# Optimization experiments

Measured on AMD Instinct MI355X. Metric: run time of the kernel, lower is better.

The kernel has to match this reference:

```python
import jax, jax.numpy as jnp
import numpy as np

N, E, IN, HID, H, G, CLS = 20000, 160000, 128, 96, 6, 512, 128
HD = H * HID  # heads * out_channels = 576
ARC_S = 30.0  # ArcFace scale (no margin at inference, no labels passed)


def _lin_params(key, fan_in, fan_out):
    k1, k2 = jax.random.split(key)
    lim = 1.0 / np.sqrt(fan_in)
    W = jax.random.uniform(k1, (fan_in, fan_out), minval=-lim, maxval=lim, dtype=jnp.float32)
    b = jax.random.uniform(k2, (fan_out,), minval=-lim, maxval=lim, dtype=jnp.float32)
    return W, b


def setup_inputs() -> dict:
    key = jax.random.key(0)
    ks = jax.random.split(key, 32)
    x = jax.random.normal(ks[0], (N, IN), dtype=jnp.float32)
    edge_index = jax.random.randint(ks[1], (2, E), 0, N, dtype=jnp.int64)
    batch = jnp.sort(jax.random.randint(ks[2], (N,), 0, G, dtype=jnp.int64))
    # conv1: IN -> HID (per-head dim HID, H heads)
    Wq1, bq1 = _lin_params(ks[3], IN, HD)
    Wk1, bk1 = _lin_params(ks[4], IN, HD)
    Wv1, bv1 = _lin_params(ks[5], IN, HD)
    Ws1, bs1 = _lin_params(ks[6], IN, HID)
    # convs 2..5 share shapes: HID -> HID, stacked on leading axis of 4
    def stack(fn_keys, fi, fo):
        Ws, bs = zip(*[_lin_params(k, fi, fo) for k in fn_keys])
        return jnp.stack(Ws), jnp.stack(bs)
    Wq_r, bq_r = stack(ks[7:11], HID, HD)
    Wk_r, bk_r = stack(ks[11:15], HID, HD)
    Wv_r, bv_r = stack(ks[15:19], HID, HD)
    Ws_r, bs_r = stack(ks[19:23], HID, HID)
    fc1_w, fc1_b = _lin_params(ks[23], HID, HID)
    fc2_w, fc2_b = _lin_params(ks[24], HID, HID)
    arc_w = jax.random.normal(ks[25], (CLS, HID), dtype=jnp.float32)
    return dict(x=x, edge_index=edge_index, batch=batch,
                Wq1=Wq1, bq1=bq1, Wk1=Wk1, bk1=bk1, Wv1=Wv1, bv1=bv1, Ws1=Ws1, bs1=bs1,
                Wq_r=Wq_r, bq_r=bq_r, Wk_r=Wk_r, bk_r=bk_r, Wv_r=Wv_r, bv_r=bv_r,
                Ws_r=Ws_r, bs_r=bs_r,
                fc1_w=fc1_w, fc1_b=fc1_b, fc2_w=fc2_w, fc2_b=fc2_b, arc_w=arc_w)


def transformer_conv(x, src, dst, Wq, bq, Wk, bk, Wv, bv, Ws, bs):
    n = x.shape[0]
    q = (x @ Wq + bq).reshape(n, H, HID)
    k = (x @ Wk + bk).reshape(n, H, HID)
    v = (x @ Wv + bv).reshape(n, H, HID)
    # edge-wise attention logits [E, H]
    alpha = jnp.einsum('ehd,ehd->eh', q[dst], k[src]) / jnp.sqrt(jnp.float32(HID))
    # segment softmax over incoming edges of each destination node
    m = jax.ops.segment_max(alpha, dst, num_segments=n)
    a = jnp.exp(alpha - m[dst])
    s = jax.ops.segment_sum(a, dst, num_segments=n)
    a = a / s[dst]
    out = jax.ops.segment_sum(a[:, :, None] * v[src], dst, num_segments=n)  # [n, H, HID]
    # concat=False -> mean over heads; root_weight skip connection
    return out.mean(axis=1) + x @ Ws + bs


def reference(x, edge_index, batch,
              Wq1, bq1, Wk1, bk1, Wv1, bv1, Ws1, bs1,
              Wq_r, bq_r, Wk_r, bk_r, Wv_r, bv_r, Ws_r, bs_r,
              fc1_w, fc1_b, fc2_w, fc2_b, arc_w):
    src, dst = edge_index[0], edge_index[1]
    h = jax.nn.relu(transformer_conv(x, src, dst, Wq1, bq1, Wk1, bk1, Wv1, bv1, Ws1, bs1))
    for i in range(4):  # gtconv2..gtconv5
        h = jax.nn.relu(transformer_conv(h, src, dst, Wq_r[i], bq_r[i], Wk_r[i], bk_r[i],
                                         Wv_r[i], bv_r[i], Ws_r[i], bs_r[i]))
    # global mean pool over graphs
    sums = jax.ops.segment_sum(h, batch, num_segments=G)
    cnt = jax.ops.segment_sum(jnp.ones((h.shape[0], 1), h.dtype), batch, num_segments=G)
    g = sums / jnp.maximum(cnt, 1.0)
    g = jax.nn.relu(g @ fc1_w + fc1_b)
    g = jax.nn.relu(g @ fc2_w + fc2_b)
    # ArcFace without labels: scaled cosine logits
    gn = g / (jnp.linalg.norm(g, axis=-1, keepdims=True) + 1e-12)
    wn = arc_w / (jnp.linalg.norm(arc_w, axis=-1, keepdims=True) + 1e-12)
    return ARC_S * (gn @ wn.T)
```

## Files before the change

### kernel.cpp

```cpp
#include <hip/hip_runtime.h>
#include <math.h>

#define N_NODES 20000
#define N_EDGES 160000
#define DIM_IN  128
#define HIDDEN  96
#define NH      6
#define HD      576
#define LDROW   704
#define KVF8LD  1152
#define NALL    1824
#define NGRAPH  512
#define NCLS    128
#define CHUNK   32
#define SLD     104
#define BSTR    112

typedef unsigned short ushort_t;
typedef unsigned char uchar_t;
typedef __attribute__((ext_vector_type(8))) short bf16x8;
typedef __attribute__((ext_vector_type(4))) float f32x4;
typedef __attribute__((ext_vector_type(2))) float f32x2;

static __device__ __forceinline__ ushort_t f2bf(float f) {
    unsigned int u = __float_as_uint(f);
    return (ushort_t)((u + 0x7fffu + ((u >> 16) & 1u)) >> 16);
}
static __device__ __forceinline__ float bfs(ushort_t u) { return __uint_as_float((unsigned int)u << 16); }
static __device__ __forceinline__ float bflo(unsigned int u) { return __uint_as_float(u << 16); }
static __device__ __forceinline__ float bfhi(unsigned int u) { return __uint_as_float(u & 0xffff0000u); }

__global__ void k_cvt(const float* __restrict__ src, ushort_t* __restrict__ dst, int n)
{
    int i = blockIdx.x * blockDim.x + threadIdx.x;
    if (i < n) dst[i] = f2bf(src[i]);
}

__global__ void k_cvt_wT_all(
    const float* __restrict__ Wq1, const float* __restrict__ Wk1,
    const float* __restrict__ Wv1, const float* __restrict__ Ws1,
    const float* __restrict__ Wq_r, const float* __restrict__ Wk_r,
    const float* __restrict__ Wv_r, const float* __restrict__ Ws_r,
    ushort_t* __restrict__ Wb0, ushort_t* __restrict__ Wbr)
{
    const int L = blockIdx.y;
    const int K = (L == 0) ? DIM_IN : HIDDEN;
    int i = blockIdx.x * blockDim.x + threadIdx.x;
    if (i >= K * NALL) return;
    const float *Wq, *Wk, *Wv, *Ws; ushort_t* dst;
    if (L == 0) { Wq = Wq1; Wk = Wk1; Wv = Wv1; Ws = Ws1; dst = Wb0; }
    else {
        int j = L - 1;
        Wq = Wq_r + (size_t)j * HIDDEN * HD; Wk = Wk_r + (size_t)j * HIDDEN * HD;
        Wv = Wv_r + (size_t)j * HIDDEN * HD; Ws = Ws_r + (size_t)j * HIDDEN * HIDDEN;
        dst = Wbr + (size_t)j * HIDDEN * NALL;
    }
    int n = i / K, k = i - n * K;
    float v;
    if (n < 576)       v = Wq[(size_t)k * HD + n];
    else if (n < 1152) v = Wk[(size_t)k * HD + (n - 576)];
    else if (n < 1728) v = Wv[(size_t)k * HD + (n - 1152)];
    else               v = Ws[(size_t)k * HIDDEN + (n - 1728)];
    dst[i] = f2bf(v);
}

template<int KDIM>
__global__ __launch_bounds__(256) void gemm_qkvs_mfma(
    const ushort_t* __restrict__ A, int M,
    const ushort_t* __restrict__ WbT,
    const float* __restrict__ bq, const float* __restrict__ bk,
    const float* __restrict__ bv, const float* __restrict__ bs,
    ushort_t* __restrict__ kvqs, uchar_t* __restrict__ kvf8)
{
    constexpr int LDB = KDIM + 8;
    constexpr int K8  = KDIM >> 3;
    __shared__ __align__(16) ushort_t smem[128 * SLD];
    const int t    = threadIdx.x;
    const int lane = t & 63;
    const int w    = t >> 6;
    const int wm   = w & 1, wn = w >> 1;
    const int quad = lane >> 4;
    const int l16  = lane & 15;
    const int m0   = blockIdx.y * 128;
    const int rb   = blockIdx.x;
    const int n0   = rb * 96;

    for (int idx = t; idx < 96 * K8; idx += 256) {
        int c = idx / K8, kc = idx - c * K8;
        uint4 v = *(const uint4*)(WbT + (size_t)(n0 + c) * KDIM + kc * 8);
        *(uint4*)(&smem[c * LDB + kc * 8]) = v;
    }

    const ushort_t* Arow[4];
    #pragma unroll
    for (int i = 0; i < 4; i++) {
        int row = m0 + wm * 64 + i * 16 + l16;
        row = min(row, M - 1);
        Arow[i] = A + (size_t)row * KDIM + quad * 8;
    }
    __syncthreads();

    f32x4 acc[4][3] = {};
    #pragma unroll
    for (int ks = 0; ks < KDIM; ks += 32) {
        bf16x8 af[4], bfv[3];
        #pragma unroll
        for (int i = 0; i < 4; i++) af[i] = *(const bf16x8*)(Arow[i] + ks);
        #pragma unroll
        for (int j = 0; j < 3; j++)
            bfv[j] = *(const bf16x8*)(&smem[(wn * 48 + j * 16 + l16) * LDB + ks + quad * 8]);
        #pragma unroll
        for (int i = 0; i < 4; i++)
            #pragma unroll
            for (int j = 0; j < 3; j++)
                acc[i][j] = __builtin_amdgcn_mfma_f32_16x16x32_bf16(af[i], bfv[j], acc[i][j], 0, 0, 0);
    }

    int region; const float* biasp;
    if (rb < 6)       { region = 0; biasp = bq; }
    else if (rb < 12) { region = 1; biasp = bk; }
    else if (rb < 18) { region = 2; biasp = bv; }
    else              { region = 3; biasp = bs; }
    const int colbase = (region == 3) ? 0 : (rb - region * 6) * 96;
    float bj[3];
    #pragma unroll
    for (int j = 0; j < 3; j++) bj[j] = biasp[colbase + wn * 48 + j * 16 + l16];

    __syncthreads();

    if (region == 1 || region == 2) {
        uchar_t* bstage = (uchar_t*)smem;
        #pragma unroll
        for (int i = 0; i < 4; i++) {
            #pragma unroll
            for (int r = 0; r < 4; r++) {
                int row = wm * 64 + i * 16 + quad * 4 + r;
                #pragma unroll
                for (int j = 0; j < 3; j++) {
                    float v = acc[i][j][r] + bj[j];
                    int pk = __builtin_amdgcn_cvt_pk_fp8_f32(v, v, 0, false);
                    bstage[row * BSTR + wn * 48 + j * 16 + l16] = (uchar_t)(pk & 0xff);
                }
            }
        }
        __syncthreads();
        const int c0 = (rb - 6) * 96;
        for (int idx = t; idx < 128 * 6; idx += 256) {
            int r = idx / 6, v4 = idx - r * 6;
            int row = m0 + r;
            if (row < M)
                *(uint4*)(kvf8 + (size_t)row * KVF8LD + c0 + v4 * 16) =
                    *(const uint4*)(bstage + r * BSTR + v4 * 16);
        }
    } else {
        int dstoff = (region == 0) ? n0 : 576;
        #pragma unroll
        for (int i = 0; i < 4; i++) {
            #pragma unroll
            for (int r = 0; r < 4; r++) {
                int row = wm * 64 + i * 16 + quad * 4 + r;
                #pragma unroll
                for (int j = 0; j < 3; j++)
                    smem[row * SLD + wn * 48 + j * 16 + l16] = f2bf(acc[i][j][r] + bj[j]);
            }
        }
        __syncthreads();
        for (int idx = t; idx < 128 * 12; idx += 256) {
            int r = idx / 12, v = idx - r * 12;
            int row = m0 + r;
            if (row < M)
                *(uint4*)(kvqs + (size_t)row * LDROW + dstoff + v * 8) =
                    *(const uint4*)(&smem[r * SLD + v * 8]);
        }
    }
}

__global__ void k_deg(const int* __restrict__ edst, int* __restrict__ deg)
{
    int e = blockIdx.x * blockDim.x + threadIdx.x;
    if (e < N_EDGES) atomicAdd(&deg[edst[e]], 1);
}

__global__ __launch_bounds__(1024) void k_scan(const int* __restrict__ deg,
                                               int* __restrict__ row_ptr,
                                               int* __restrict__ cursor)
{
    __shared__ int part[1024];
    int t = threadIdx.x;
    const int chunk = (N_NODES + 1023) / 1024;
    int b = t * chunk;
    int s = 0;
    for (int i = 0; i < chunk; i++)
        if (b + i < N_NODES) s += deg[b + i];
    part[t] = s;
    __syncthreads();
    for (int o = 1; o < 1024; o <<= 1) {
        int v = (t >= o) ? part[t - o] : 0;
        __syncthreads();
        part[t] += v;
        __syncthreads();
    }
    int run = part[t] - s;
    for (int i = 0; i < chunk; i++) {
        if (b + i < N_NODES) {
            row_ptr[b + i] = run;
            cursor[b + i]  = run;
            run += deg[b + i];
        }
    }
    if (t == 1023) row_ptr[N_NODES] = part[1023];
}

__global__ void k_scatter(const int* __restrict__ esrc, const int* __restrict__ edst,
                          int* __restrict__ cursor, int* __restrict__ csrc)
{
    int e = blockIdx.x * blockDim.x + threadIdx.x;
    if (e < N_EDGES) {
        int pos = atomicAdd(&cursor[edst[e]], 1);
        csrc[pos] = esrc[e];
    }
}

__global__ void k_gbound(const int* __restrict__ batch, int* __restrict__ gbound)
{
    int g = blockIdx.x * blockDim.x + threadIdx.x;
    if (g > NGRAPH) return;
    int lo = 0, hi = N_NODES;
    while (lo < hi) {
        int mid = (lo + hi) >> 1;
        if (batch[mid] < g) lo = mid + 1; else hi = mid;
    }
    gbound[g] = lo;
}

__global__ __launch_bounds__(192) void node_attn(
    const ushort_t* __restrict__ kvqs, const uchar_t* __restrict__ kvf8,
    const int* __restrict__ row_ptr, const int* __restrict__ csrc,
    ushort_t* __restrict__ hb, float* __restrict__ hf)
{
    const int n = blockIdx.x;
    const int t = threadIdx.x;
    const int lane = t & 31;
    const int g = t >> 5;
    const int el = lane >> 2;
    const int qr = lane & 3;

    __shared__ float Qs[HD];
    __shared__ float wbuf[CHUNK * NH];
    __shared__ int   srcs[CHUNK];
    __shared__ float m[NH], l[NH], scale[NH], linv[NH];
    __shared__ float arr[HD];

    const int beg = row_ptr[n], end = row_ptr[n + 1];
    const ushort_t* qk = kvqs + (size_t)n * LDROW;

    if (t < 72) {
        uint4 v = *(const uint4*)(qk + t * 8);
        unsigned int uu[4] = {v.x, v.y, v.z, v.w};
        #pragma unroll
        for (int j = 0; j < 4; j++) {
            Qs[t * 8 + 2 * j]     = bflo(uu[j]);
            Qs[t * 8 + 2 * j + 1] = bfhi(uu[j]);
        }
    }
    if (t < NH) { m[t] = -1e30f; l[t] = 0.f; }

    const int d4 = 4 * t;
    const int hh = d4 / HIDDEN;
    float a[4] = {0.f, 0.f, 0.f, 0.f};
    const float qa = 0.10206207261596577f;
    const uchar_t* vbase = kvf8 + 576 + d4;

    for (int cb = beg; cb < end; cb += CHUNK) {
        const int c = min(CHUNK, end - cb);
        __syncthreads();
        if (t < c) srcs[t] = csrc[cb + t];
        __syncthreads();

        for (int eb = 0; eb < c; eb += 8) {
            int e8 = eb + el;
            bool act = e8 < c;
            int src = srcs[act ? e8 : 0];
            const uchar_t* kp = kvf8 + (size_t)src * KVF8LD + g * HIDDEN + qr * 24;
            uint2 a0 = *(const uint2*)(kp);
            uint2 a1 = *(const uint2*)(kp + 8);
            uint2 a2 = *(const uint2*)(kp + 16);
            const float* qb = &Qs[g * HIDDEN + qr * 24];
            unsigned int uu[6] = {a0.x, a0.y, a1.x, a1.y, a2.x, a2.y};
            float p = 0.f;
            #pragma unroll
            for (int k2 = 0; k2 < 6; k2++) {
                f32x2 lo = __builtin_amdgcn_cvt_pk_f32_fp8(uu[k2], false);
                f32x2 hi = __builtin_amdgcn_cvt_pk_f32_fp8(uu[k2], true);
                p += lo[0] * qb[4 * k2]     + lo[1] * qb[4 * k2 + 1]
                   + hi[0] * qb[4 * k2 + 2] + hi[1] * qb[4 * k2 + 3];
            }
            p += __shfl_xor(p, 1, 32);
            p += __shfl_xor(p, 2, 32);
            if (act && qr == 0) wbuf[e8 * NH + g] = p * qa;
        }
        __syncthreads();

        {
            float logit = (lane < c) ? wbuf[lane * NH + g] : -1e30f;
            float cm = logit;
            #pragma unroll
            for (int o = 16; o; o >>= 1) cm = fmaxf(cm, __shfl_xor(cm, o, 32));
            cm = fmaxf(cm, m[g]);
            float wv = (lane < c) ? __expf(logit - cm) : 0.f;
            if (lane < c) wbuf[lane * NH + g] = wv;
            float lp = wv;
            #pragma unroll
            for (int o = 16; o; o >>= 1) lp += __shfl_xor(lp, o, 32);
            if (lane == 0) {
                float sc = __expf(m[g] - cm);
                scale[g] = sc;
                l[g] = l[g] * sc + lp;
                m[g] = cm;
            }
        }
        __syncthreads();

        if (t < 144) {
            float sc = scale[hh];
            #pragma unroll
            for (int j = 0; j < 4; j++) a[j] *= sc;
            int e = 0;
            for (; e + 4 <= c; e += 4) {
                unsigned int r[4];
                #pragma unroll
                for (int j = 0; j < 4; j++)
                    r[j] = *(const unsigned int*)(vbase + (size_t)srcs[e + j] * KVF8LD);
                #pragma unroll
                for (int j = 0; j < 4; j++) {
                    float w2 = wbuf[(e + j) * NH + hh];
                    f32x2 lo = __builtin_amdgcn_cvt_pk_f32_fp8(r[j], false);
                    f32x2 hi = __builtin_amdgcn_cvt_pk_f32_fp8(r[j], true);
                    a[0] += w2 * lo[0];
                    a[1] += w2 * lo[1];
                    a[2] += w2 * hi[0];
                    a[3] += w2 * hi[1];
                }
            }
            for (; e < c; e++) {
                unsigned int r = *(const unsigned int*)(vbase + (size_t)srcs[e] * KVF8LD);
                float w2 = wbuf[e * NH + hh];
                f32x2 lo = __builtin_amdgcn_cvt_pk_f32_fp8(r, false);
                f32x2 hi = __builtin_amdgcn_cvt_pk_f32_fp8(r, true);
                a[0] += w2 * lo[0];
                a[1] += w2 * lo[1];
                a[2] += w2 * hi[0];
                a[3] += w2 * hi[1];
            }
        }
    }

    if (t < NH) linv[t] = (l[t] > 0.f) ? 1.0f / l[t] : 0.f;
    __syncthreads();
    if (t < 144) {
        float li = linv[hh];
        #pragma unroll
        for (int j = 0; j < 4; j++) arr[d4 + j] = a[j] * li;
    }
    __syncthreads();

    if (t < HIDDEN) {
        float s = (arr[t] + arr[HIDDEN + t] + arr[2 * HIDDEN + t] +
                   arr[3 * HIDDEN + t] + arr[4 * HIDDEN + t] + arr[5 * HIDDEN + t])
                  * (1.0f / 6.0f);
        s += bfs(qk[576 + t]);
        s = fmaxf(s, 0.0f);
        hb[n * HIDDEN + t] = f2bf(s);
        hf[n * HIDDEN + t] = s;
    }
}

__global__ __launch_bounds__(128) void k_head(
    const float* __restrict__ hf, const int* __restrict__ gbound,
    const float* __restrict__ fc1w, const float* __restrict__ fc1b,
    const float* __restrict__ fc2w, const float* __restrict__ fc2b,
    const float* __restrict__ arcw, float* __restrict__ out)
{
    int g = blockIdx.x, t = threadIdx.x;
    __shared__ float v0[HIDDEN], v1[HIDDEN], v2[HIDDEN];
    __shared__ float gnorm;
    const int s0 = gbound[g], s1 = gbound[g + 1];
    float cnt = fmaxf((float)(s1 - s0), 1.0f);
    if (t < HIDDEN) {
        float s = 0.f;
        for (int n = s0; n < s1; n++) s += hf[(size_t)n * HIDDEN + t];
        v0[t] = s / cnt;
    }
    __syncthreads();
    if (t < HIDDEN) {
        float s = fc1b[t];
        for (int k = 0; k < HIDDEN; k++) s += v0[k] * fc1w[k * HIDDEN + t];
        v1[t] = fmaxf(s, 0.f);
    }
    __syncthreads();
    if (t < HIDDEN) {
        float s = fc2b[t];
        for (int k = 0; k < HIDDEN; k++) s += v1[k] * fc2w[k * HIDDEN + t];
        v2[t] = fmaxf(s, 0.f);
    }
    __syncthreads();
    if (t == 0) {
        float s = 0.f;
        for (int k = 0; k < HIDDEN; k++) s += v2[k] * v2[k];
        gnorm = sqrtf(s) + 1e-12f;
    }
    __syncthreads();
    if (t < NCLS) {
        float dot = 0.f, wn = 0.f;
        const float* wr = arcw + (size_t)t * HIDDEN;
        for (int k = 0; k < HIDDEN; k++) {
            float w = wr[k];
            dot += w * v2[k];
            wn  += w * w;
        }
        out[g * NCLS + t] = 30.0f * dot / (gnorm * (sqrtf(wn) + 1e-12f));
    }
}

extern "C" void kernel_launch(void* const* d_in, const int* in_sizes, int n_in,
                              void* d_out, int out_size, void* d_ws, size_t ws_size,
                              hipStream_t stream)
{
    (void)in_sizes; (void)n_in; (void)out_size; (void)ws_size;

    const float* x     = (const float*)d_in[0];
    const int*   ei    = (const int*)d_in[1];
    const int*   batch = (const int*)d_in[2];
    const float* Wq1 = (const float*)d_in[3];  const float* bq1 = (const float*)d_in[4];
    const float* Wk1 = (const float*)d_in[5];  const float* bk1 = (const float*)d_in[6];
    const float* Wv1 = (const float*)d_in[7];  const float* bv1 = (const float*)d_in[8];
    const float* Ws1 = (const float*)d_in[9];  const float* bs1 = (const float*)d_in[10];
    const float* Wq_r = (const float*)d_in[11]; const float* bq_r = (const float*)d_in[12];
    const float* Wk_r = (const float*)d_in[13]; const float* bk_r = (const float*)d_in[14];
    const float* Wv_r = (const float*)d_in[15]; const float* bv_r = (const float*)d_in[16];
    const float* Ws_r = (const float*)d_in[17]; const float* bs_r = (const float*)d_in[18];
    const float* fc1w = (const float*)d_in[19]; const float* fc1b = (const float*)d_in[20];
    const float* fc2w = (const float*)d_in[21]; const float* fc2b = (const float*)d_in[22];
    const float* arcw = (const float*)d_in[23];
    float* out = (float*)d_out;

    const int* esrc = ei;
    const int* edst = ei + N_EDGES;

    char* base = (char*)d_ws;
    size_t off = 0;
    auto alloc = [&](size_t bytes) -> void* {
        off = (off + 255) & ~(size_t)255;
        void* p = base + off;
        off += bytes;
        return p;
    };
    ushort_t* kvqs = (ushort_t*)alloc((size_t)N_NODES * LDROW * 2);
    uchar_t*  kvf8 = (uchar_t*)alloc((size_t)N_NODES * KVF8LD);
    ushort_t* xb  = (ushort_t*)alloc((size_t)N_NODES * DIM_IN * 2);
    ushort_t* hb0 = (ushort_t*)alloc((size_t)N_NODES * HIDDEN * 2);
    ushort_t* hb1 = (ushort_t*)alloc((size_t)N_NODES * HIDDEN * 2);
    float*    hf  = (float*)alloc((size_t)N_NODES * HIDDEN * 4);
    ushort_t* Wb0 = (ushort_t*)alloc((size_t)DIM_IN * NALL * 2);
    ushort_t* Wbr = (ushort_t*)alloc((size_t)4 * HIDDEN * NALL * 2);
    int*   deg     = (int*)alloc(N_NODES * 4);
    int*   row_ptr = (int*)alloc((N_NODES + 1) * 4);
    int*   cursor  = (int*)alloc(N_NODES * 4);
    int*   csrc    = (int*)alloc(N_EDGES * 4);
    int*   gbound  = (int*)alloc((NGRAPH + 1) * 4);

    k_cvt<<<(N_NODES * DIM_IN + 255) / 256, 256, 0, stream>>>(x, xb, N_NODES * DIM_IN);
    {
        dim3 gw((DIM_IN * NALL + 255) / 256, 5);
        k_cvt_wT_all<<<gw, 256, 0, stream>>>(Wq1, Wk1, Wv1, Ws1,
                                             Wq_r, Wk_r, Wv_r, Ws_r, Wb0, Wbr);
    }

    hipMemsetAsync(deg, 0, N_NODES * 4, stream);
    k_deg<<<(N_EDGES + 255) / 256, 256, 0, stream>>>(edst, deg);
    k_scan<<<1, 1024, 0, stream>>>(deg, row_ptr, cursor);
    k_scatter<<<(N_EDGES + 255) / 256, 256, 0, stream>>>(esrc, edst, cursor, csrc);
    k_gbound<<<(NGRAPH + 1 + 255) / 256, 256, 0, stream>>>(batch, gbound);

    const ushort_t* Ain = xb;
    ushort_t* hbcur = hb0;
    for (int L = 0; L < 5; L++) {
        const ushort_t* Wb = (L == 0) ? Wb0 : (Wbr + (size_t)(L - 1) * HIDDEN * NALL);
        const float *bq, *bk, *bv, *bs;
        if (L == 0) { bq = bq1; bk = bk1; bv = bv1; bs = bs1; }
        else {
            int i = L - 1;
            bq = bq_r + (size_t)i * HD; bk = bk_r + (size_t)i * HD;
            bv = bv_r + (size_t)i * HD; bs = bs_r + (size_t)i * HIDDEN;
        }
        dim3 g(19, (N_NODES + 127) / 128);
        if (L == 0)
            gemm_qkvs_mfma<DIM_IN><<<g, 256, 0, stream>>>(Ain, N_NODES, Wb,
                                                          bq, bk, bv, bs, kvqs, kvf8);
        else
            gemm_qkvs_mfma<HIDDEN><<<g, 256, 0, stream>>>(Ain, N_NODES, Wb,
                                                          bq, bk, bv, bs, kvqs, kvf8);
        node_attn<<<N_NODES, 192, 0, stream>>>(kvqs, kvf8, row_ptr, csrc, hbcur, hf);
        Ain = hbcur;
        hbcur = (hbcur == hb0) ? hb1 : hb0;
    }

    k_head<<<NGRAPH, 128, 0, stream>>>(hf, gbound, fc1w, fc1b, fc2w, fc2b, arcw, out);
}
```

Before: 530.7 us.

## Fuse prep kernels, prefetch first V rows, drop fp32 hidden output

Merges the x-to-bf16 conversion, degree counting and graph-boundary search into one launch to cut launch overhead. In node_attn, the first eight V rows of each chunk are loaded before the logit/softmax phase so their latency overlaps with that work. The extra fp32 copy of every layer's hidden output is dropped, and the pooling head now reads the bf16 buffer instead. This saves write bandwidth in every layer but pools from bf16-rounded values, and the prefetch adds register pressure.

Result: no change. 526.6 us (-0.8%).

```diff
diff --git a/kernel.cpp b/kernel.cpp
--- a/kernel.cpp
+++ b/kernel.cpp
@@ -30,10 +30,31 @@
 static __device__ __forceinline__ float bflo(unsigned int u) { return __uint_as_float(u << 16); }
 static __device__ __forceinline__ float bfhi(unsigned int u) { return __uint_as_float(u & 0xffff0000u); }
 
-__global__ void k_cvt(const float* __restrict__ src, ushort_t* __restrict__ dst, int n)
-{
-    int i = blockIdx.x * blockDim.x + threadIdx.x;
-    if (i < n) dst[i] = f2bf(src[i]);
+#define PREP_CVT_BLOCKS 10000
+#define PREP_DEG_BLOCKS 625
+#define PREP_GB_BLOCKS  3
+__global__ void k_prep(const float* __restrict__ x, ushort_t* __restrict__ xb,
+                       const int* __restrict__ edst, int* __restrict__ deg,
+                       const int* __restrict__ batch, int* __restrict__ gbound)
+{
+    int b = blockIdx.x;
+    if (b < PREP_CVT_BLOCKS) {
+        int i = b * 256 + threadIdx.x;
+        if (i < N_NODES * DIM_IN) xb[i] = f2bf(x[i]);
+    } else if (b < PREP_CVT_BLOCKS + PREP_DEG_BLOCKS) {
+        int e = (b - PREP_CVT_BLOCKS) * 256 + threadIdx.x;
+        if (e < N_EDGES) atomicAdd(&deg[edst[e]], 1);
+    } else {
+        int g = (b - PREP_CVT_BLOCKS - PREP_DEG_BLOCKS) * 256 + threadIdx.x;
+        if (g <= NGRAPH) {
+            int lo = 0, hi = N_NODES;
+            while (lo < hi) {
+                int mid = (lo + hi) >> 1;
+                if (batch[mid] < g) lo = mid + 1; else hi = mid;
+            }
+            gbound[g] = lo;
+        }
+    }
 }
 
 __global__ void k_cvt_wT_all(
@@ -175,12 +196,6 @@
     }
 }
 
-__global__ void k_deg(const int* __restrict__ edst, int* __restrict__ deg)
-{
-    int e = blockIdx.x * blockDim.x + threadIdx.x;
-    if (e < N_EDGES) atomicAdd(&deg[edst[e]], 1);
-}
-
 __global__ __launch_bounds__(1024) void k_scan(const int* __restrict__ deg,
                                                int* __restrict__ row_ptr,
                                                int* __restrict__ cursor)
@@ -221,22 +236,10 @@
     }
 }
 
-__global__ void k_gbound(const int* __restrict__ batch, int* __restrict__ gbound)
-{
-    int g = blockIdx.x * blockDim.x + threadIdx.x;
-    if (g > NGRAPH) return;
-    int lo = 0, hi = N_NODES;
-    while (lo < hi) {
-        int mid = (lo + hi) >> 1;
-        if (batch[mid] < g) lo = mid + 1; else hi = mid;
-    }
-    gbound[g] = lo;
-}
-
 __global__ __launch_bounds__(192) void node_attn(
     const ushort_t* __restrict__ kvqs, const uchar_t* __restrict__ kvf8,
     const int* __restrict__ row_ptr, const int* __restrict__ csrc,
-    ushort_t* __restrict__ hb, float* __restrict__ hf)
+    ushort_t* __restrict__ hb)
 {
     const int n = blockIdx.x;
     const int t = threadIdx.x;
@@ -276,6 +279,15 @@
         __syncthreads();
         if (t < c) srcs[t] = csrc[cb + t];
         __syncthreads();
+
+        unsigned int vpre[8];
+        if (t < 144) {
+            #pragma unroll
+            for (int j = 0; j < 8; j++) {
+                int e = min(j, c - 1);
+                vpre[j] = *(const unsigned int*)(vbase + (size_t)srcs[e] * KVF8LD);
+            }
+        }
 
         for (int eb = 0; eb < c; eb += 8) {
             int e8 = eb + el;
@@ -325,7 +337,19 @@
             float sc = scale[hh];
             #pragma unroll
             for (int j = 0; j < 4; j++) a[j] *= sc;
-            int e = 0;
+            #pragma unroll
+            for (int j = 0; j < 8; j++) {
+                if (j < c) {
+                    float w2 = wbuf[j * NH + hh];
+                    f32x2 lo = __builtin_amdgcn_cvt_pk_f32_fp8(vpre[j], false);
+                    f32x2 hi = __builtin_amdgcn_cvt_pk_f32_fp8(vpre[j], true);
+                    a[0] += w2 * lo[0];
+                    a[1] += w2 * lo[1];
+                    a[2] += w2 * hi[0];
+                    a[3] += w2 * hi[1];
+                }
+            }
+            int e = 8;
             for (; e + 4 <= c; e += 4) {
                 unsigned int r[4];
                 #pragma unroll
@@ -371,12 +395,11 @@
         s += bfs(qk[576 + t]);
         s = fmaxf(s, 0.0f);
         hb[n * HIDDEN + t] = f2bf(s);
-        hf[n * HIDDEN + t] = s;
     }
 }
 
 __global__ __launch_bounds__(128) void k_head(
-    const float* __restrict__ hf, const int* __restrict__ gbound,
+    const ushort_t* __restrict__ hb, const int* __restrict__ gbound,
     const float* __restrict__ fc1w, const float* __restrict__ fc1b,
     const float* __restrict__ fc2w, const float* __restrict__ fc2b,
     const float* __restrict__ arcw, float* __restrict__ out)
@@ -388,7 +411,7 @@
     float cnt = fmaxf((float)(s1 - s0), 1.0f);
     if (t < HIDDEN) {
         float s = 0.f;
-        for (int n = s0; n < s1; n++) s += hf[(size_t)n * HIDDEN + t];
+        for (int n = s0; n < s1; n++) s += bfs(hb[(size_t)n * HIDDEN + t]);
         v0[t] = s / cnt;
     }
     __syncthreads();
@@ -460,7 +483,6 @@
     ushort_t* xb  = (ushort_t*)alloc((size_t)N_NODES * DIM_IN * 2);
     ushort_t* hb0 = (ushort_t*)alloc((size_t)N_NODES * HIDDEN * 2);
     ushort_t* hb1 = (ushort_t*)alloc((size_t)N_NODES * HIDDEN * 2);
-    float*    hf  = (float*)alloc((size_t)N_NODES * HIDDEN * 4);
     ushort_t* Wb0 = (ushort_t*)alloc((size_t)DIM_IN * NALL * 2);
     ushort_t* Wbr = (ushort_t*)alloc((size_t)4 * HIDDEN * NALL * 2);
     int*   deg     = (int*)alloc(N_NODES * 4);
@@ -469,18 +491,16 @@
     int*   csrc    = (int*)alloc(N_EDGES * 4);
     int*   gbound  = (int*)alloc((NGRAPH + 1) * 4);
 
-    k_cvt<<<(N_NODES * DIM_IN + 255) / 256, 256, 0, stream>>>(x, xb, N_NODES * DIM_IN);
+    hipMemsetAsync(deg, 0, N_NODES * 4, stream);
+    k_prep<<<PREP_CVT_BLOCKS + PREP_DEG_BLOCKS + PREP_GB_BLOCKS, 256, 0, stream>>>(
+        x, xb, edst, deg, batch, gbound);
     {
         dim3 gw((DIM_IN * NALL + 255) / 256, 5);
         k_cvt_wT_all<<<gw, 256, 0, stream>>>(Wq1, Wk1, Wv1, Ws1,
                                              Wq_r, Wk_r, Wv_r, Ws_r, Wb0, Wbr);
     }
-
-    hipMemsetAsync(deg, 0, N_NODES * 4, stream);
-    k_deg<<<(N_EDGES + 255) / 256, 256, 0, stream>>>(edst, deg);
     k_scan<<<1, 1024, 0, stream>>>(deg, row_ptr, cursor);
     k_scatter<<<(N_EDGES + 255) / 256, 256, 0, stream>>>(esrc, edst, cursor, csrc);
-    k_gbound<<<(NGRAPH + 1 + 255) / 256, 256, 0, stream>>>(batch, gbound);
 
     const ushort_t* Ain = xb;
     ushort_t* hbcur = hb0;
@@ -500,10 +520,11 @@
         else
             gemm_qkvs_mfma<HIDDEN><<<g, 256, 0, stream>>>(Ain, N_NODES, Wb,
                                                           bq, bk, bv, bs, kvqs, kvf8);
-        node_attn<<<N_NODES, 192, 0, stream>>>(kvqs, kvf8, row_ptr, csrc, hbcur, hf);
+        node_attn<<<N_NODES, 192, 0, stream>>>(kvqs, kvf8, row_ptr, csrc, hbcur);
         Ain = hbcur;
         hbcur = (hbcur == hb0) ? hb1 : hb0;
     }
 
-    k_head<<<NGRAPH, 128, 0, stream>>>(hf, gbound, fc1w, fc1b, fc2w, fc2b, arcw, out);
-}
+    k_head<<<NGRAPH, 128, 0, stream>>>(hbcur == hb0 ? hb1 : hb0, gbound,
+                                       fc1w, fc1b, fc2w, fc2b, arcw, out);
+}
```
